# Kernel optimization log

Measured on AMD Instinct MI355X. Metric: run time of the kernel, lower is better.

## Reference

```python
import jax, jax.numpy as jnp
import numpy as np

B, S, H, NH, HD, ROT = 4, 1024, 2048, 16, 128, 64
P = NH * HD  # attention projection size = 2048
EPS = 1e-6


def setup_inputs() -> dict:
    key = jax.random.key(0)
    ks = jax.random.split(key, 12)
    T = B * S
    # rotary frequency table [max_pos=S, 1, ROT]
    inv_freq = 1.0 / (10000.0 ** (np.arange(0, ROT, 2, dtype=np.float32) / ROT))
    f = np.outer(np.arange(S, dtype=np.float32), inv_freq)  # [S, ROT/2]
    freqs = np.concatenate([f, f], axis=-1)[:, None, :].astype(np.float32)
    sc = 0.02
    return {
        "positions": jnp.tile(jnp.arange(S, dtype=jnp.int64), B),  # per-seq positions 0..S-1
        "hidden_states": jax.random.normal(ks[0], (T, H), jnp.float32),
        "rotary_pos_emb": jnp.asarray(freqs),
        "lf1_cache": jax.random.normal(ks[1], (B, 1, H), jnp.float32) * sc,
        "lf2_cache": jax.random.normal(ks[2], (B, 1, H // 2), jnp.float32) * sc,
        "Wqk": jax.random.normal(ks[3], (2 * P, H), jnp.float32) * sc,
        "Wv": jax.random.normal(ks[4], (P, H), jnp.float32) * sc,
        "Wo": jax.random.normal(ks[5], (H, P), jnp.float32) * sc,
        "conv1_w": jax.random.normal(ks[6], (H // 2, H, 2), jnp.float32) * sc,  # [out, in, tap]
        "conv1_b": jnp.zeros((H // 2,), jnp.float32),
        "conv2_w": jax.random.normal(ks[7], (H, H // 2, 2), jnp.float32) * sc,
        "conv2_b": jnp.zeros((H,), jnp.float32),
        "ln_g": jnp.ones((H,), jnp.float32),
    }


def reference(positions, hidden_states, rotary_pos_emb, lf1_cache, lf2_cache,
              Wqk, Wv, Wo, conv1_w, conv1_b, conv2_w, conv2_b, ln_g):
    T = hidden_states.shape[0]
    scaling = HD ** -0.5

    # v projection on raw hidden states (done before lf_gate in the source)
    v = hidden_states @ Wv.T  # [T, P]

    # ---- LocalizedFiltering (two causal 2-tap convs + residual + RMSNorm),
    # vectorized over all sequences (source loops per sequence) ----
    x = hidden_states.reshape(B, S, H)
    xc = jnp.concatenate([lf1_cache, x], axis=1)  # [B, S+1, H]
    o1 = (jnp.einsum('bsh,oh->bso', xc[:, :-1], conv1_w[..., 0])
          + jnp.einsum('bsh,oh->bso', xc[:, 1:], conv1_w[..., 1]) + conv1_b)  # [B,S,H/2]
    o1c = jnp.concatenate([lf2_cache, o1], axis=1)  # [B, S+1, H/2]
    o2 = (jnp.einsum('bsc,oc->bso', o1c[:, :-1], conv2_w[..., 0])
          + jnp.einsum('bsc,oc->bso', o1c[:, 1:], conv2_w[..., 1]) + conv2_b)  # [B,S,H]
    o3 = o2 + x
    lf = o3 * jax.lax.rsqrt(jnp.mean(o3 * o3, axis=-1, keepdims=True) + EPS) * ln_g

    hs = lf.reshape(T, H)
    qk = (hs @ Wqk.T).reshape(T, NH, 2 * HD)
    q, k = jnp.split(qk, 2, axis=-1)  # each [T, NH, HD]

    # partial rotary (mscale = 1.0 since use_yarn=False)
    f = rotary_pos_emb[positions]            # [T, 1, ROT]
    cos, sin = jnp.cos(f), jnp.sin(f)

    def rope(t):
        tr, tp = t[..., :ROT], t[..., ROT:]
        t1, t2 = jnp.split(tr, 2, axis=-1)
        rot = jnp.concatenate([-t2, t1], axis=-1)
        return jnp.concatenate([tr * cos + rot * sin, tp], axis=-1)

    qb = rope(q).reshape(B, S, NH, HD)
    kb = rope(k).reshape(B, S, NH, HD)
    vb = v.reshape(B, S, NH, HD)

    # causal attention per sequence
    scores = jnp.einsum('bqhd,bkhd->bhqk', qb, kb) * scaling
    mask = jnp.tril(jnp.ones((S, S), bool))
    scores = jnp.where(mask, scores, jnp.finfo(scores.dtype).min)
    attn = jax.nn.softmax(scores, axis=-1)
    out = jnp.einsum('bhqk,bkhd->bqhd', attn, vb).reshape(T, P)
    return out @ Wo.T  # [T, H]
```

## Files before the change

### kernel.cpp

```cpp
#include <hip/hip_runtime.h>

typedef __bf16 bf16;
typedef __bf16 bf16x8 __attribute__((ext_vector_type(8)));
typedef __bf16 bf16x4 __attribute__((ext_vector_type(4)));
typedef float f32x4 __attribute__((ext_vector_type(4)));
typedef float f32x2 __attribute__((ext_vector_type(2)));

#define DEVI __device__ __forceinline__

constexpr int Bc = 4, Sc = 1024, Hc = 2048, NHc = 16, HDc = 128;
constexpr int Tc = Bc * Sc;
constexpr int Pc = NHc * HDc;

DEVI void async16(const void* g, void* l) {
  __builtin_amdgcn_global_load_lds(
      (const __attribute__((address_space(1))) unsigned int*)g,
      (__attribute__((address_space(3))) unsigned int*)l, 16, 0, 0);
}

#define BAR() __builtin_amdgcn_s_barrier()
#define LGKM0()                                          \
  do {                                                   \
    asm volatile("s_waitcnt lgkmcnt(0)" ::: "memory");   \
    __builtin_amdgcn_sched_barrier(0);                   \
  } while (0)
#define VM0() asm volatile("s_waitcnt vmcnt(0)" ::: "memory")

template <int WM, int WN, int MREP, int NREP, int EPI>
__global__ __launch_bounds__(512, 2) void gemm8(
    const bf16* __restrict__ A, const bf16* __restrict__ W,
    void* __restrict__ C0, void* __restrict__ C1,
    const float* __restrict__ biasf, const f32x2* __restrict__ cst,
    int M, int N, int K) {
  constexpr int BM = WM * MREP * 16;
  constexpr int BN = WN * NREP * 16;
  constexpr int MH = MREP / 2, NH = NREP / 2;
  constexpr int LA = BM / 128;
  constexpr int LB = BN / 128;
  constexpr int STG = (BM + BN) * 128;
  constexpr int OUTB = (EPI == 3) ? 4 : 2;
  constexpr int CBYTES = BM * BN * OUTB;
  constexpr int LDSB = (2 * STG > CBYTES) ? 2 * STG : CBYTES;
  __shared__ char lds[LDSB];

  const int nbx = N / BN;
  const int nwg = (M / BM) * nbx;
  const int wgid = (blockIdx.x & 7) * (nwg >> 3) + (blockIdx.x >> 3);
  const int bx = wgid % nbx, by = wgid / nbx;
  const int m0 = by * BM, n0 = bx * BN;
  const int tid = threadIdx.x;
  const int w = tid >> 6, l = tid & 63;
  const int wm = w / WN, wn = w % WN;
  const int lr = l & 15, hi = l >> 4;

  auto vminf = [&] {
    constexpr int LL = LA + LB;
    if constexpr (LL == 4)      asm volatile("s_waitcnt vmcnt(4)" ::: "memory");
    else if constexpr (LL == 3) asm volatile("s_waitcnt vmcnt(3)" ::: "memory");
    else if constexpr (LL == 2) asm volatile("s_waitcnt vmcnt(2)" ::: "memory");
    else                        asm volatile("s_waitcnt vmcnt(0)" ::: "memory");
  };

  auto stageA = [&](int buf, int t, int half) {
#pragma unroll
    for (int c = 0; c < LA; ++c) {
      const int ch = c * 512 + tid;
      const int row = half * (BM / 2) + (ch >> 3);
      const int grp = ch & 7;
      async16(A + (size_t)(m0 + row) * K + (t << 6) + ((grp ^ (row & 7)) << 3),
              &lds[buf * STG + row * 128 + grp * 16]);
    }
  };
  auto stageB = [&](int buf, int t, int half) {
#pragma unroll
    for (int c = 0; c < LB; ++c) {
      const int ch = c * 512 + tid;
      const int row = half * (BN / 2) + (ch >> 3);
      const int grp = ch & 7;
      async16(W + (size_t)(n0 + row) * K + (t << 6) + ((grp ^ (row & 7)) << 3),
              &lds[buf * STG + BM * 128 + row * 128 + grp * 16]);
    }
  };
  auto LD = [&](const char* Lp, int row, int g) -> bf16x8 {
    return *(const bf16x8*)(Lp + ((size_t)row << 7) + ((g ^ (row & 7)) << 4));
  };

#define QUAD(MB_, NB_, FB_)                                                     \
  do {                                                                          \
    __builtin_amdgcn_s_setprio(1);                                              \
    _Pragma("unroll") for (int m = 0; m < MH; ++m)                              \
      _Pragma("unroll") for (int n = 0; n < NH; ++n)                            \
        _Pragma("unroll") for (int kk = 0; kk < 2; ++kk)                        \
          acc[(MB_) + m][(NB_) + n] = __builtin_amdgcn_mfma_f32_16x16x32_bf16(  \
              fa[m][kk], FB_[n][kk], acc[(MB_) + m][(NB_) + n], 0, 0, 0);       \
    __builtin_amdgcn_s_setprio(0);                                              \
  } while (0)

  f32x4 acc[MREP][NREP] = {};
  bf16x8 fa[MH][2], fb0[NH][2], fb1[NH][2];
  const int nk = K >> 6;

  stageA(0, 0, 0);
  stageB(0, 0, 0);
  stageA(0, 0, 1);
  stageB(0, 0, 1);
  stageA(1, 1, 0);
  stageB(1, 1, 0);
  vminf();
  BAR();

#pragma unroll 1
  for (int t = 0; t < nk; ++t) {
    const char* Lb = &lds[(t & 1) * STG];
    const int cur = t & 1, nbuf = cur ^ 1;
    const bool pf1 = (t + 1 < nk);
#pragma unroll
    for (int m = 0; m < MH; ++m) {
      const int r = wm * (MREP * 16) + m * 16 + lr;
      fa[m][0] = LD(Lb, r, hi);
      fa[m][1] = LD(Lb, r, 4 + hi);
    }
#pragma unroll
    for (int n = 0; n < NH; ++n) {
      const int r = BM + wn * (NREP * 16) + n * 16 + lr;
      fb0[n][0] = LD(Lb, r, hi);
      fb0[n][1] = LD(Lb, r, 4 + hi);
    }
    if (pf1) stageA(nbuf, t + 1, 1);
    BAR();
    LGKM0();
    QUAD(0, 0, fb0);
    BAR();
#pragma unroll
    for (int n = 0; n < NH; ++n) {
      const int r = BM + wn * (NREP * 16) + (NH + n) * 16 + lr;
      fb1[n][0] = LD(Lb, r, hi);
      fb1[n][1] = LD(Lb, r, 4 + hi);
    }
    if (pf1) stageB(nbuf, t + 1, 1);
    BAR();
    LGKM0();
    QUAD(0, NH, fb1);
    BAR();
#pragma unroll
    for (int m = 0; m < MH; ++m) {
      const int r = wm * (MREP * 16) + (MH + m) * 16 + lr;
      fa[m][0] = LD(Lb, r, hi);
      fa[m][1] = LD(Lb, r, 4 + hi);
    }
    BAR();
    LGKM0();
    QUAD(MH, NH, fb1);
    BAR();
    QUAD(MH, 0, fb0);
    if (t + 2 < nk) {
      stageA(cur, t + 2, 0);
      stageB(cur, t + 2, 0);
      vminf();
    } else {
      VM0();
    }
    BAR();
  }
#undef QUAD

  if constexpr (EPI == 0) {
    bf16* cl = (bf16*)lds;
#pragma unroll
    for (int mi = 0; mi < MREP; ++mi)
#pragma unroll
      for (int ni = 0; ni < NREP; ++ni) {
        const int col = wn * (NREP * 16) + ni * 16 + lr;
        const float bv = biasf ? biasf[n0 + col] : 0.f;
#pragma unroll
        for (int j = 0; j < 4; ++j) {
          const int row = wm * (MREP * 16) + mi * 16 + (hi << 2) + j;
          cl[row * BN + ((((col >> 3) ^ (row & 7)) << 3) | (col & 7))] =
              (bf16)(acc[mi][ni][j] + bv);
        }
      }
    __syncthreads();
    constexpr int GPR = BN / 8;
    constexpr int PT = BM * GPR / 512;
#pragma unroll
    for (int c = 0; c < PT; ++c) {
      const int ch = c * 512 + tid;
      const int row = ch / GPR, g = ch % GPR;
      bf16x8 vv = *(const bf16x8*)&cl[row * BN + ((g ^ (row & 7)) << 3)];
      *(bf16x8*)&((bf16*)C0)[(size_t)(m0 + row) * N + n0 + g * 8] = vv;
    }
  } else if constexpr (EPI == 1) {
    bf16* cl = (bf16*)lds;
#pragma unroll
    for (int mi = 0; mi < MREP; ++mi)
#pragma unroll
      for (int ni = 0; ni < NREP; ++ni) {
        const int col = wn * (NREP * 16) + ni * 16 + lr;
#pragma unroll
        for (int j = 0; j < 4; ++j) {
          const int row = wm * (MREP * 16) + mi * 16 + (hi << 2) + j;
          cl[col * BM + ((((row >> 3) ^ (col & 7)) << 3) | (row & 7))] =
              (bf16)acc[mi][ni][j];
        }
      }
    __syncthreads();
    const int s0 = m0 & 1023, bq = m0 >> 10;
    bf16* vT = (bf16*)C0;
    const size_t vbase = (((size_t)(bq * 16 + (n0 >> 7)) * 128) << 10) + s0;
    constexpr int GPR = BM / 8;
    constexpr int PT = BN * GPR / 512;
#pragma unroll
    for (int c = 0; c < PT; ++c) {
      const int ch = c * 512 + tid;
      const int d = ch / GPR, g = ch % GPR;
      bf16x8 vv = *(const bf16x8*)&cl[d * BM + ((g ^ (d & 7)) << 3)];
      *(bf16x8*)&vT[vbase + ((size_t)d << 10) + g * 8] = vv;
    }
  } else if constexpr (EPI == 2) {
    bf16* cl = (bf16*)lds;
#pragma unroll
    for (int mi = 0; mi < MREP; ++mi)
#pragma unroll
      for (int ni = 0; ni < NREP; ++ni) {
        const int col = wn * (NREP * 16) + ni * 16 + lr;
#pragma unroll
        for (int j = 0; j < 4; ++j) {
          const int row = wm * (MREP * 16) + mi * 16 + (hi << 2) + j;
          cl[row * BN + ((((col >> 3) ^ (row & 7)) << 3) | (col & 7))] =
              (bf16)acc[mi][ni][j];
        }
      }
    __syncthreads();
    const int s0 = m0 & 1023, bq = m0 >> 10, head = n0 >> 8;
    bf16* qr = (bf16*)C0;
    bf16* kr = (bf16*)C1;
    const size_t qbase = ((size_t)((bq * 16 + head) * 1024 + s0) << 7);
    constexpr int GPR = BN / 8;
    constexpr int PT = BM * GPR / 512;
#pragma unroll
    for (int c = 0; c < PT; ++c) {
      const int ch = c * 512 + tid;
      const int row = ch / GPR, g = ch % GPR;
      const int cc = g * 8;
      const int isk = cc >> 7, dd = cc & 127;
      bf16x8 vv = *(const bf16x8*)&cl[row * BN + ((g ^ (row & 7)) << 3)];
      bf16x8 out;
      if (dd < 64) {
        bf16x8 pp = *(const bf16x8*)&cl[row * BN + (((g ^ 4) ^ (row & 7)) << 3)];
        const f32x2* cp = &cst[(s0 + row) * 64 + dd];
#pragma unroll
        for (int e = 0; e < 8; ++e) {
          const f32x2 cs = cp[e];
          const float pv = (dd < 32) ? -(float)pp[e] : (float)pp[e];
          out[e] = (bf16)((float)vv[e] * cs[0] + pv * cs[1]);
        }
      } else {
        out = vv;
      }
      bf16* dst = isk ? kr : qr;
      *(bf16x8*)&dst[qbase + ((size_t)row << 7) + dd] = out;
    }
  } else {
    float* cl = (float*)lds;
#pragma unroll
    for (int mi = 0; mi < MREP; ++mi)
#pragma unroll
      for (int ni = 0; ni < NREP; ++ni) {
        const int col = wn * (NREP * 16) + ni * 16 + lr;
        const float bv = biasf ? biasf[n0 + col] : 0.f;
#pragma unroll
        for (int j = 0; j < 4; ++j) {
          const int row = wm * (MREP * 16) + mi * 16 + (hi << 2) + j;
          cl[row * BN + ((((col >> 2) ^ (row & 7)) << 2) | (col & 3))] =
              acc[mi][ni][j] + bv;
        }
      }
    __syncthreads();
    constexpr int GPR = BN / 4;
    constexpr int PT = BM * GPR / 512;
#pragma unroll
    for (int c = 0; c < PT; ++c) {
      const int ch = c * 512 + tid;
      const int row = ch / GPR, g = ch % GPR;
      f32x4 vv = *(const f32x4*)&cl[row * BN + ((g ^ (row & 7)) << 2)];
      *(f32x4*)&((float*)C0)[(size_t)(m0 + row) * N + n0 + g * 4] = vv;
    }
  }
}

template <int WM, int WN, int MREP, int NREP>
__global__ __launch_bounds__(WM * WN * 64, 2) void gemm_pipe(
    const bf16* __restrict__ A, const bf16* __restrict__ W, void* __restrict__ Cout,
    const float* __restrict__ bias, int M, int N, int K) {
  constexpr int BM = WM * MREP * 16;
  constexpr int BN = WN * NREP * 16;
  constexpr int THREADS = WM * WN * 64;
  constexpr int ROWS = BM + BN;
  constexpr int CHA = BM * 4 / THREADS;
  constexpr int CHB = BN * 4 / THREADS;
  static_assert(CHA + CHB == 4, "vmcnt ledger assumes 4 loads/thread/stage");
  __shared__ bf16 lds[4][ROWS * 32];
  static_assert(BM * BN * 2 <= sizeof(lds), "C tile must fit LDS for epilogue");

  const int nbx = N / BN;
  const int nwg = (M / BM) * nbx;
  const int wgid = (blockIdx.x & 7) * (nwg >> 3) + (blockIdx.x >> 3);
  const int bx = wgid % nbx, by = wgid / nbx;
  const int m0 = by * BM, n0 = bx * BN;
  const int tid = threadIdx.x;
  const int w = tid >> 6, l = tid & 63;
  const int wm = w / WN, wn = w % WN;
  const int lr = l & 15;
  const int hi = l >> 4;

  auto stage = [&](int slot, int t) {
    const int k0 = t << 5;
#pragma unroll
    for (int c = 0; c < CHA; ++c) {
      const int ch = c * THREADS + tid;
      const int row = ch >> 2, cg = ch & 3;
      const int gc = (cg ^ ((row >> 1) & 3)) << 3;
      async16(A + (size_t)(m0 + row) * K + k0 + gc, (char*)&lds[slot][0] + ch * 16);
    }
#pragma unroll
    for (int c = 0; c < CHB; ++c) {
      const int ch = c * THREADS + tid;
      const int row = ch >> 2, cg = ch & 3;
      const int gc = (cg ^ ((row >> 1) & 3)) << 3;
      async16(W + (size_t)(n0 + row) * K + k0 + gc,
              (char*)&lds[slot][0] + (BM * 4 + ch) * 16);
    }
  };

  f32x4 acc[MREP][NREP] = {};
  const int nk = K >> 5;

  stage(0, 0);
  stage(1, 1);
  stage(2, 2);
  asm volatile("s_waitcnt vmcnt(8)" ::: "memory");
  __builtin_amdgcn_s_barrier();
  __builtin_amdgcn_sched_barrier(0);

  bf16x8 fAc[MREP], fBc[NREP], fAn[MREP], fBn[NREP];
  {
    const char* nb = (const char*)&lds[0][0];
#pragma unroll
    for (int mi = 0; mi < MREP; ++mi) {
      const int r = wm * (MREP * 16) + mi * 16 + lr;
      fAc[mi] = *(const bf16x8*)(nb + r * 64 + ((hi ^ ((r >> 1) & 3)) << 4));
    }
#pragma unroll
    for (int ni = 0; ni < NREP; ++ni) {
      const int r = BM + wn * (NREP * 16) + ni * 16 + lr;
      fBc[ni] = *(const bf16x8*)(nb + r * 64 + ((hi ^ ((r >> 1) & 3)) << 4));
    }
  }

#define GSTEP(T_, CA, CB, NA, NB)                                              \
  do {                                                                         \
    if ((T_) + 2 < nk) asm volatile("s_waitcnt vmcnt(4)" ::: "memory");        \
    else               asm volatile("s_waitcnt vmcnt(0)" ::: "memory");        \
    __builtin_amdgcn_s_barrier();                                              \
    __builtin_amdgcn_sched_barrier(0);                                         \
    if ((T_) + 3 < nk) stage(((T_) + 3) & 3, (T_) + 3);                        \
    if ((T_) + 1 < nk) {                                                       \
      const char* nb = (const char*)&lds[((T_) + 1) & 3][0];                   \
      _Pragma("unroll") for (int mi = 0; mi < MREP; ++mi) {                    \
        const int r = wm * (MREP * 16) + mi * 16 + lr;                         \
        NA[mi] = *(const bf16x8*)(nb + r * 64 + ((hi ^ ((r >> 1) & 3)) << 4)); \
      }                                                                        \
      _Pragma("unroll") for (int ni = 0; ni < NREP; ++ni) {                    \
        const int r = BM + wn * (NREP * 16) + ni * 16 + lr;                    \
        NB[ni] = *(const bf16x8*)(nb + r * 64 + ((hi ^ ((r >> 1) & 3)) << 4)); \
      }                                                                        \
    }                                                                          \
    __builtin_amdgcn_s_setprio(1);                                             \
    _Pragma("unroll") for (int mi = 0; mi < MREP; ++mi)                        \
      _Pragma("unroll") for (int ni = 0; ni < NREP; ++ni)                      \
        acc[mi][ni] =                                                          \
            __builtin_amdgcn_mfma_f32_16x16x32_bf16(CA[mi], CB[ni], acc[mi][ni], 0, 0, 0); \
    __builtin_amdgcn_s_setprio(0);                                             \
  } while (0)

  for (int t = 0; t < nk; t += 2) {
    GSTEP(t, fAc, fBc, fAn, fBn);
    GSTEP(t + 1, fAn, fBn, fAc, fBc);
  }
#undef GSTEP

  __syncthreads();
  {
    bf16* cl = (bf16*)&lds[0][0];
#pragma unroll
    for (int mi = 0; mi < MREP; ++mi) {
#pragma unroll
      for (int ni = 0; ni < NREP; ++ni) {
        const int col = wn * (NREP * 16) + ni * 16 + lr;
        const float bv = bias ? bias[n0 + col] : 0.f;
#pragma unroll
        for (int j = 0; j < 4; ++j) {
          const int row = wm * (MREP * 16) + mi * 16 + (hi << 2) + j;
          cl[row * BN + ((((col >> 3) ^ (row & 7)) << 3) | (col & 7))] =
              (bf16)(acc[mi][ni][j] + bv);
        }
      }
    }
    __syncthreads();
    constexpr int GPR = BN / 8;
    constexpr int PT = BM * GPR / THREADS;
#pragma unroll
    for (int c = 0; c < PT; ++c) {
      const int ch = c * THREADS + tid;
      const int row = ch / GPR, g = ch % GPR;
      bf16x8 vv = *(const bf16x8*)&cl[row * BN + ((g ^ (row & 7)) << 3)];
      *(bf16x8*)&((bf16*)Cout)[(size_t)(m0 + row) * N + n0 + g * 8] = vv;
    }
  }
}

__global__ void k_f2b4(const float* __restrict__ in, bf16* __restrict__ out, int n4) {
  int i = blockIdx.x * 256 + threadIdx.x;
  if (i >= n4) return;
  float4 v = ((const float4*)in)[i];
  bf16x4 o = {(bf16)v.x, (bf16)v.y, (bf16)v.z, (bf16)v.w};
  ((bf16x4*)out)[i] = o;
}

__global__ void k_trig(const float* __restrict__ rot, f32x2* __restrict__ cst) {
  int i = blockIdx.x * 256 + threadIdx.x;
  float f = rot[i];
  f32x2 cs = {cosf(f), sinf(f)};
  cst[i] = cs;
}

__global__ void k_build_a1(const float* __restrict__ hid, const float* __restrict__ lf1,
                           bf16* __restrict__ hsb, bf16* __restrict__ A1) {
  int idx = blockIdx.x * 256 + threadIdx.x;
  int t = idx >> 11, h = idx & 2047;
  float x = hid[idx];
  hsb[idx] = (bf16)x;
  float xp;
  if ((t & (Sc - 1)) == 0)
    xp = lf1[(t >> 10) * Hc + h];
  else
    xp = hid[idx - Hc];
  size_t a = ((size_t)t << 12) + 2 * h;
  A1[a] = (bf16)xp;
  A1[a + 1] = (bf16)x;
}

__global__ void k_build_a2(const bf16* __restrict__ o1, const float* __restrict__ lf2,
                           bf16* __restrict__ A2) {
  int idx = blockIdx.x * 256 + threadIdx.x;
  int t = idx >> 10, c = idx & 1023;
  bf16 cur = o1[idx];
  bf16 prev;
  if ((t & (Sc - 1)) == 0)
    prev = (bf16)lf2[(t >> 10) * 1024 + c];
  else
    prev = o1[idx - 1024];
  size_t a = ((size_t)t << 11) + 2 * c;
  A2[a] = prev;
  A2[a + 1] = cur;
}

__global__ __launch_bounds__(256) void k_rmsnorm(const bf16* __restrict__ o2,
                                                 const float* __restrict__ hid,
                                                 const float* __restrict__ g,
                                                 bf16* __restrict__ lf) {
  int t = blockIdx.x, tid = threadIdx.x;
  size_t base = ((size_t)t << 11) + tid * 8;
  bf16x8 ov = *(const bf16x8*)&o2[base];
  const float* hp = &hid[base];
  float vals[8];
  float ss = 0.f;
#pragma unroll
  for (int i = 0; i < 8; ++i) {
    float x = (float)ov[i] + hp[i];
    vals[i] = x;
    ss += x * x;
  }
#pragma unroll
  for (int off = 1; off < 64; off <<= 1) ss += __shfl_xor(ss, off);
  __shared__ float red[4];
  if ((tid & 63) == 0) red[tid >> 6] = ss;
  __syncthreads();
  float tot = red[0] + red[1] + red[2] + red[3];
  float inv = rsqrtf(tot * (1.f / 2048.f) + 1e-6f);
  bf16x8 o;
#pragma unroll
  for (int i = 0; i < 8; ++i) o[i] = (bf16)(vals[i] * inv * g[tid * 8 + i]);
  *(bf16x8*)&lf[base] = o;
}

__global__ __launch_bounds__(256, 2) void k_attn(const bf16* __restrict__ qr,
                                                 const bf16* __restrict__ kr,
                                                 const bf16* __restrict__ vT,
                                                 bf16* __restrict__ att) {
  __shared__ bf16 Ks[2][64 * 128];
  __shared__ bf16 Vs[2][128 * 64];
  __shared__ bf16 plds[4][16 * 64];
  const int bid = blockIdx.x;
  const int xcd = bid & 7, jj = bid >> 3;
  const int bn = xcd * 8 + (jj >> 3);
  const int pr = jj & 7;
  const int tid = threadIdx.x, w = tid >> 6, l = tid & 63;
  const int lr = l & 15, hi = l >> 4;
  const bf16* kb = kr + ((size_t)bn << 17);
  const bf16* vb = vT + ((size_t)bn << 17);
  const int b = bn >> 4, hh = bn & 15;
  const float scaling = 0.08838834764831845f;

  auto stage = [&](int buf, int kt) {
#pragma unroll
    for (int c = 0; c < 4; ++c) {
      int chunk = c * 256 + tid;
      int prow = chunk >> 4, pcg = chunk & 15;
      async16(kb + ((size_t)(kt * 64 + prow) << 7) + ((pcg ^ (prow & 7)) << 3),
              (char*)&Ks[buf][0] + chunk * 16);
    }
#pragma unroll
    for (int c = 0; c < 4; ++c) {
      int chunk = c * 256 + tid;
      int prow = chunk >> 3, pcg = chunk & 7;
      async16(vb + ((size_t)prow << 10) + kt * 64 + ((pcg ^ (prow & 7)) << 3),
              (char*)&Vs[buf][0] + chunk * 16);
    }
  };

#pragma unroll 1
  for (int phase = 0; phase < 2; ++phase) {
    const int qt = phase ? (15 - pr) : pr;
    const int qg0 = qt * 64 + w * 16;
    const bf16* qb = qr + ((size_t)(bn * 1024 + qg0) << 7);
    bf16x8 qf[4];
#pragma unroll
    for (int ks = 0; ks < 4; ++ks) qf[ks] = *(const bf16x8*)&qb[lr * 128 + ks * 32 + hi * 8];
    f32x4 oacc[8] = {};
    float mrow[4] = {-1e30f, -1e30f, -1e30f, -1e30f};
    float lrow[4] = {0.f, 0.f, 0.f, 0.f};
    const int nkb = qt + 1;

    stage(0, 0);
    __syncthreads();

    for (int kbt = 0; kbt < nkb; ++kbt) {
      const int cur = kbt & 1;
      if (kbt + 1 < nkb) stage(cur ^ 1, kbt + 1);

      f32x4 sacc[4] = {};
#pragma unroll
      for (int n = 0; n < 4; ++n) {
        const int krow = n * 16 + lr;
#pragma unroll
        for (int ks = 0; ks < 4; ++ks) {
          bf16x8 kf = *(const bf16x8*)&Ks[cur][(krow << 7) + ((((ks << 2) | hi) ^ (krow & 7)) << 3)];
          sacc[n] = __builtin_amdgcn_mfma_f32_16x16x32_bf16(qf[ks], kf, sacc[n], 0, 0, 0);
        }
      }
      const bool needmask = (kbt * 64 + 63 > qg0);
#pragma unroll
      for (int n = 0; n < 4; ++n) {
        int kg = kbt * 64 + n * 16 + lr;
#pragma unroll
        for (int j = 0; j < 4; ++j) {
          float sv = sacc[n][j] * scaling;
          if (needmask && kg > qg0 + hi * 4 + j) sv = -1e30f;
          sacc[n][j] = sv;
        }
      }
      float sf[4];
#pragma unroll
      for (int j = 0; j < 4; ++j) {
        float pm = fmaxf(fmaxf(sacc[0][j], sacc[1][j]), fmaxf(sacc[2][j], sacc[3][j]));
        pm = fmaxf(pm, __shfl_xor(pm, 1));
        pm = fmaxf(pm, __shfl_xor(pm, 2));
        pm = fmaxf(pm, __shfl_xor(pm, 4));
        pm = fmaxf(pm, __shfl_xor(pm, 8));
        float mn = fmaxf(mrow[j], pm);
        sf[j] = __expf(mrow[j] - mn);
        mrow[j] = mn;
      }
#pragma unroll
      for (int n = 0; n < 4; ++n)
#pragma unroll
        for (int j = 0; j < 4; ++j) sacc[n][j] = __expf(sacc[n][j] - mrow[j]);
#pragma unroll
      for (int j = 0; j < 4; ++j) {
        float ps = sacc[0][j] + sacc[1][j] + sacc[2][j] + sacc[3][j];
        ps += __shfl_xor(ps, 1);
        ps += __shfl_xor(ps, 2);
        ps += __shfl_xor(ps, 4);
        ps += __shfl_xor(ps, 8);
        lrow[j] = lrow[j] * sf[j] + ps;
      }
#pragma unroll
      for (int dt = 0; dt < 8; ++dt)
#pragma unroll
        for (int j = 0; j < 4; ++j) oacc[dt][j] *= sf[j];
#pragma unroll
      for (int n = 0; n < 4; ++n)
#pragma unroll
        for (int j = 0; j < 4; ++j)
          plds[w][(hi * 4 + j) * 64 + n * 16 + lr] = (bf16)sacc[n][j];
      asm volatile("s_waitcnt lgkmcnt(0)" ::: "memory");
#pragma unroll
      for (int ks2 = 0; ks2 < 2; ++ks2) {
        bf16x8 pf = *(const bf16x8*)&plds[w][lr * 64 + ks2 * 32 + hi * 8];
#pragma unroll
        for (int dt = 0; dt < 8; ++dt) {
          const int vrow = dt * 16 + lr;
          bf16x8 vf = *(const bf16x8*)&Vs[cur][(vrow << 6) + ((((ks2 << 2) | hi) ^ (lr & 7)) << 3)];
          oacc[dt] = __builtin_amdgcn_mfma_f32_16x16x32_bf16(pf, vf, oacc[dt], 0, 0, 0);
        }
      }
      __syncthreads();
    }

#pragma unroll
    for (int j = 0; j < 4; ++j) {
      float inv = 1.f / lrow[j];
      int qg = qg0 + hi * 4 + j;
      size_t obase = ((size_t)(b * 1024 + qg) << 11) + hh * 128;
#pragma unroll
      for (int dt = 0; dt < 8; ++dt) att[obase + dt * 16 + lr] = (bf16)(oacc[dt][j] * inv);
    }
  }
}

extern "C" void kernel_launch(void* const* d_in, const int* in_sizes, int n_in,
                              void* d_out, int out_size, void* d_ws, size_t ws_size,
                              hipStream_t stream) {
  const float* hid = (const float*)d_in[1];
  const float* rot = (const float*)d_in[2];
  const float* lf1 = (const float*)d_in[3];
  const float* lf2 = (const float*)d_in[4];
  const float* Wqk = (const float*)d_in[5];
  const float* Wv  = (const float*)d_in[6];
  const float* Wo  = (const float*)d_in[7];
  const float* c1w = (const float*)d_in[8];
  const float* c1b = (const float*)d_in[9];
  const float* c2w = (const float*)d_in[10];
  const float* c2b = (const float*)d_in[11];
  const float* lng = (const float*)d_in[12];
  float* outp = (float*)d_out;
  char* ws = (char*)d_ws;

  const size_t MB = 1ull << 20;
  bf16* Wslot = (bf16*)(ws + 0 * MB);
  bf16* A1    = (bf16*)(ws + 16 * MB);
  bf16* qr    = (bf16*)(ws + 16 * MB);
  bf16* kr    = (bf16*)(ws + 32 * MB);
  bf16* hsb   = (bf16*)(ws + 48 * MB);
  bf16* lfb   = hsb;
  bf16* vT    = (bf16*)(ws + 64 * MB);
  bf16* o1    = (bf16*)(ws + 80 * MB);
  bf16* A2    = (bf16*)(ws + 88 * MB);
  bf16* att   = A2;
  bf16* o2    = (bf16*)(ws + 104 * MB);
  f32x2* cst  = (f32x2*)(ws + 120 * MB);

  auto f2b = [&](const float* in, bf16* out, int n) {
    int n4 = n / 4;
    k_f2b4<<<(n4 + 255) / 256, 256, 0, stream>>>(in, out, n4);
  };

  k_trig<<<Sc * 64 / 256, 256, 0, stream>>>(rot, cst);

  f2b(Wv, Wslot, 2048 * 2048);
  k_build_a1<<<Tc * Hc / 256, 256, 0, stream>>>(hid, lf1, hsb, A1);
  gemm8<4, 2, 4, 4, 1><<<256, 512, 0, stream>>>(hsb, Wslot, vT, nullptr, nullptr, nullptr,
                                                Tc, Pc, Hc);

  f2b(c1w, Wslot, 1024 * 2048 * 2);
  gemm_pipe<2, 2, 4, 4><<<256, 256, 0, stream>>>(A1, Wslot, o1, c1b, Tc, 1024, 4096);

  k_build_a2<<<Tc * 1024 / 256, 256, 0, stream>>>(o1, lf2, A2);
  f2b(c2w, Wslot, 2048 * 1024 * 2);
  gemm8<4, 2, 4, 4, 0><<<256, 512, 0, stream>>>(A2, Wslot, o2, nullptr, c2b, nullptr,
                                                Tc, 2048, 2048);

  k_rmsnorm<<<Tc, 256, 0, stream>>>(o2, hid, lng, lfb);

  f2b(Wqk, Wslot, 4096 * 2048);
  gemm8<2, 4, 8, 4, 2><<<256, 512, 0, stream>>>(lfb, Wslot, qr, kr, nullptr, cst,
                                                Tc, 4096, Hc);

  k_attn<<<Bc * NHc * 8, 256, 0, stream>>>(qr, kr, vT, att);

  f2b(Wo, Wslot, 2048 * 2048);
  gemm8<4, 2, 4, 4, 3><<<256, 512, 0, stream>>>(att, Wslot, outp, nullptr, nullptr, nullptr,
                                                Tc, 2048, 2048);
}
```

Before: 354.0 us.

## Read conv taps from padded activations instead of materialized interleaved im2col buffers

Removes the k_build_a1/k_build_a2 kernels that wrote interleaved [prev,cur] im2col copies. Activations are now stored in a per-sequence padded layout (S+1 rows with the cache row first), and the conv GEMMs address tap 0 and tap 1 as two K halves of shifted rows. Conv weights are de-interleaved into tap-major order to match. The first conv GEMM writes straight into the padded o1 buffer. A new XCD-aware tile mapping for 256-tile gemm8 grids is also added. This saves several large memory passes at the cost of more complex address arithmetic in the A loads.

```diff
diff --git a/kernel.cpp b/kernel.cpp
--- a/kernel.cpp
+++ b/kernel.cpp
@@ -3,6 +3,7 @@
 typedef __bf16 bf16;
 typedef __bf16 bf16x8 __attribute__((ext_vector_type(8)));
 typedef __bf16 bf16x4 __attribute__((ext_vector_type(4)));
+typedef __bf16 bf16x2 __attribute__((ext_vector_type(2)));
 typedef float f32x4 __attribute__((ext_vector_type(4)));
 typedef float f32x2 __attribute__((ext_vector_type(2)));
 
@@ -11,6 +12,7 @@
 constexpr int Bc = 4, Sc = 1024, Hc = 2048, NHc = 16, HDc = 128;
 constexpr int Tc = Bc * Sc;
 constexpr int Pc = NHc * HDc;
+constexpr int SP = Sc + 1;
 
 DEVI void async16(const void* g, void* l) {
   __builtin_amdgcn_global_load_lds(
@@ -26,7 +28,7 @@
   } while (0)
 #define VM0() asm volatile("s_waitcnt vmcnt(0)" ::: "memory")
 
-template <int WM, int WN, int MREP, int NREP, int EPI>
+template <int WM, int WN, int MREP, int NREP, int EPI, int AMODE>
 __global__ __launch_bounds__(512, 2) void gemm8(
     const bf16* __restrict__ A, const bf16* __restrict__ W,
     void* __restrict__ C0, void* __restrict__ C1,
@@ -45,8 +47,16 @@
 
   const int nbx = N / BN;
   const int nwg = (M / BM) * nbx;
-  const int wgid = (blockIdx.x & 7) * (nwg >> 3) + (blockIdx.x >> 3);
-  const int bx = wgid % nbx, by = wgid / nbx;
+  int bx, by;
+  if (nwg == 256 && nbx == 16) {
+    const int xcd = blockIdx.x & 7, loc = blockIdx.x >> 3;
+    by = (xcd >> 1) * 4 + (loc >> 3);
+    bx = (xcd & 1) * 8 + (loc & 7);
+  } else {
+    const int wgid = (blockIdx.x & 7) * (nwg >> 3) + (blockIdx.x >> 3);
+    bx = wgid % nbx;
+    by = wgid / nbx;
+  }
   const int m0 = by * BM, n0 = bx * BN;
   const int tid = threadIdx.x;
   const int w = tid >> 6, l = tid & 63;
@@ -61,13 +71,27 @@
     else                        asm volatile("s_waitcnt vmcnt(0)" ::: "memory");
   };
 
+  auto aAddr = [&](int row, int t) -> const bf16* {
+    const int m = m0 + row;
+    if constexpr (AMODE == 0) {
+      return A + (size_t)m * K + (t << 6);
+    } else if constexpr (AMODE == 1) {
+      return A + (size_t)((m >> 10) * SP + (m & 1023) + 1) * K + (t << 6);
+    } else {
+      const int Kh2 = K >> 1, nkh = Kh2 >> 6;
+      const int tap = (t >= nkh) ? 1 : 0;
+      return A + (size_t)((m >> 10) * SP + (m & 1023) + tap) * Kh2 +
+             ((t - (tap ? nkh : 0)) << 6);
+    }
+  };
+
   auto stageA = [&](int buf, int t, int half) {
 #pragma unroll
     for (int c = 0; c < LA; ++c) {
       const int ch = c * 512 + tid;
       const int row = half * (BM / 2) + (ch >> 3);
       const int grp = ch & 7;
-      async16(A + (size_t)(m0 + row) * K + (t << 6) + ((grp ^ (row & 7)) << 3),
+      async16(aAddr(row, t) + ((grp ^ (row & 7)) << 3),
               &lds[buf * STG + row * 128 + grp * 16]);
     }
   };
@@ -288,7 +312,7 @@
   }
 }
 
-template <int WM, int WN, int MREP, int NREP>
+template <int WM, int WN, int MREP, int NREP, int AMODE, bool OUTPAD>
 __global__ __launch_bounds__(WM * WN * 64, 2) void gemm_pipe(
     const bf16* __restrict__ A, const bf16* __restrict__ W, void* __restrict__ Cout,
     const float* __restrict__ bias, int M, int N, int K) {
@@ -313,6 +337,18 @@
   const int lr = l & 15;
   const int hi = l >> 4;
 
+  auto aAddr = [&](int row, int t) -> const bf16* {
+    const int m = m0 + row;
+    if constexpr (AMODE == 2) {
+      const int Kh2 = K >> 1, nkh = Kh2 >> 5;
+      const int tap = (t >= nkh) ? 1 : 0;
+      return A + (size_t)((m >> 10) * SP + (m & 1023) + tap) * Kh2 +
+             ((t - (tap ? nkh : 0)) << 5);
+    } else {
+      return A + (size_t)m * K + (t << 5);
+    }
+  };
+
   auto stage = [&](int slot, int t) {
     const int k0 = t << 5;
 #pragma unroll
@@ -320,7 +356,7 @@
       const int ch = c * THREADS + tid;
       const int row = ch >> 2, cg = ch & 3;
       const int gc = (cg ^ ((row >> 1) & 3)) << 3;
-      async16(A + (size_t)(m0 + row) * K + k0 + gc, (char*)&lds[slot][0] + ch * 16);
+      async16(aAddr(row, t) + gc, (char*)&lds[slot][0] + ch * 16);
     }
 #pragma unroll
     for (int c = 0; c < CHB; ++c) {
@@ -413,8 +449,11 @@
     for (int c = 0; c < PT; ++c) {
       const int ch = c * THREADS + tid;
       const int row = ch / GPR, g = ch % GPR;
+      const int mr = m0 + row;
+      const size_t orow = OUTPAD ? (size_t)((mr >> 10) * SP + (mr & 1023) + 1)
+                                 : (size_t)mr;
       bf16x8 vv = *(const bf16x8*)&cl[row * BN + ((g ^ (row & 7)) << 3)];
-      *(bf16x8*)&((bf16*)Cout)[(size_t)(m0 + row) * N + n0 + g * 8] = vv;
+      *(bf16x8*)&((bf16*)Cout)[orow * N + n0 + g * 8] = vv;
     }
   }
 }
@@ -427,6 +466,18 @@
   ((bf16x4*)out)[i] = o;
 }
 
+__global__ void k_deint(const float* __restrict__ in, bf16* __restrict__ out,
+                        int O, int Hd) {
+  int i = blockIdx.x * 256 + threadIdx.x;
+  if (i >= O * (Hd >> 1)) return;
+  int o = i / (Hd >> 1), h0 = (i % (Hd >> 1)) * 2;
+  float4 v = *(const float4*)&in[(size_t)o * Hd * 2 + h0 * 2];
+  bf16x2 t0 = {(bf16)v.x, (bf16)v.z};
+  bf16x2 t1 = {(bf16)v.y, (bf16)v.w};
+  *(bf16x2*)&out[(size_t)o * 2 * Hd + h0] = t0;
+  *(bf16x2*)&out[(size_t)o * 2 * Hd + Hd + h0] = t1;
+}
+
 __global__ void k_trig(const float* __restrict__ rot, f32x2* __restrict__ cst) {
   int i = blockIdx.x * 256 + threadIdx.x;
   float f = rot[i];
@@ -434,35 +485,21 @@
   cst[i] = cs;
 }
 
-__global__ void k_build_a1(const float* __restrict__ hid, const float* __restrict__ lf1,
-                           bf16* __restrict__ hsb, bf16* __restrict__ A1) {
+__global__ void k_build_hsbp(const float* __restrict__ hid, const float* __restrict__ lf1,
+                             const float* __restrict__ lf2,
+                             bf16* __restrict__ hsbp, bf16* __restrict__ o1p) {
   int idx = blockIdx.x * 256 + threadIdx.x;
   int t = idx >> 11, h = idx & 2047;
-  float x = hid[idx];
-  hsb[idx] = (bf16)x;
-  float xp;
-  if ((t & (Sc - 1)) == 0)
-    xp = lf1[(t >> 10) * Hc + h];
-  else
-    xp = hid[idx - Hc];
-  size_t a = ((size_t)t << 12) + 2 * h;
-  A1[a] = (bf16)xp;
-  A1[a + 1] = (bf16)x;
-}
-
-__global__ void k_build_a2(const bf16* __restrict__ o1, const float* __restrict__ lf2,
-                           bf16* __restrict__ A2) {
-  int idx = blockIdx.x * 256 + threadIdx.x;
-  int t = idx >> 10, c = idx & 1023;
-  bf16 cur = o1[idx];
-  bf16 prev;
-  if ((t & (Sc - 1)) == 0)
-    prev = (bf16)lf2[(t >> 10) * 1024 + c];
-  else
-    prev = o1[idx - 1024];
-  size_t a = ((size_t)t << 11) + 2 * c;
-  A2[a] = prev;
-  A2[a + 1] = cur;
+  int b = t >> 10, s = t & 1023;
+  hsbp[((size_t)(b * SP + s + 1) << 11) + h] = (bf16)hid[idx];
+  if (idx < Bc * Hc) {
+    int bb = idx >> 11, hh = idx & 2047;
+    hsbp[((size_t)(bb * SP) << 11) + hh] = (bf16)lf1[idx];
+  }
+  if (idx < Bc * 1024) {
+    int bb = idx >> 10, cc = idx & 1023;
+    o1p[((size_t)(bb * SP) << 10) + cc] = (bf16)lf2[idx];
+  }
 }
 
 __global__ __launch_bounds__(256) void k_rmsnorm(const bf16* __restrict__ o2,
@@ -649,17 +686,15 @@
 
   const size_t MB = 1ull << 20;
   bf16* Wslot = (bf16*)(ws + 0 * MB);
-  bf16* A1    = (bf16*)(ws + 16 * MB);
-  bf16* qr    = (bf16*)(ws + 16 * MB);
-  bf16* kr    = (bf16*)(ws + 32 * MB);
-  bf16* hsb   = (bf16*)(ws + 48 * MB);
-  bf16* lfb   = hsb;
-  bf16* vT    = (bf16*)(ws + 64 * MB);
-  bf16* o1    = (bf16*)(ws + 80 * MB);
-  bf16* A2    = (bf16*)(ws + 88 * MB);
-  bf16* att   = A2;
-  bf16* o2    = (bf16*)(ws + 104 * MB);
-  f32x2* cst  = (f32x2*)(ws + 120 * MB);
+  bf16* hsbp  = (bf16*)(ws + 16 * MB);
+  bf16* att   = (bf16*)(ws + 16 * MB);
+  bf16* o1p   = (bf16*)(ws + 34 * MB);
+  bf16* o2    = (bf16*)(ws + 43 * MB);
+  bf16* lfb   = (bf16*)(ws + 59 * MB);
+  bf16* vT    = (bf16*)(ws + 75 * MB);
+  bf16* qr    = (bf16*)(ws + 91 * MB);
+  bf16* kr    = (bf16*)(ws + 107 * MB);
+  f32x2* cst  = (f32x2*)(ws + 123 * MB);
 
   auto f2b = [&](const float* in, bf16* out, int n) {
     int n4 = n / 4;
@@ -667,29 +702,29 @@
   };
 
   k_trig<<<Sc * 64 / 256, 256, 0, stream>>>(rot, cst);
+  k_build_hsbp<<<Tc * Hc / 256, 256, 0, stream>>>(hid, lf1, lf2, hsbp, o1p);
 
   f2b(Wv, Wslot, 2048 * 2048);
-  k_build_a1<<<Tc * Hc / 256, 256, 0, stream>>>(hid, lf1, hsb, A1);
-  gemm8<4, 2, 4, 4, 1><<<256, 512, 0, stream>>>(hsb, Wslot, vT, nullptr, nullptr, nullptr,
-                                                Tc, Pc, Hc);
-
-  f2b(c1w, Wslot, 1024 * 2048 * 2);
-  gemm_pipe<2, 2, 4, 4><<<256, 256, 0, stream>>>(A1, Wslot, o1, c1b, Tc, 1024, 4096);
-
-  k_build_a2<<<Tc * 1024 / 256, 256, 0, stream>>>(o1, lf2, A2);
-  f2b(c2w, Wslot, 2048 * 1024 * 2);
-  gemm8<4, 2, 4, 4, 0><<<256, 512, 0, stream>>>(A2, Wslot, o2, nullptr, c2b, nullptr,
-                                                Tc, 2048, 2048);
+  gemm8<4, 2, 4, 4, 1, 1><<<256, 512, 0, stream>>>(hsbp, Wslot, vT, nullptr, nullptr,
+                                                   nullptr, Tc, Pc, Hc);
+
+  k_deint<<<(1024 * 1024 + 255) / 256, 256, 0, stream>>>(c1w, Wslot, 1024, 2048);
+  gemm_pipe<2, 2, 4, 4, 2, true><<<256, 256, 0, stream>>>(hsbp, Wslot, o1p, c1b,
+                                                          Tc, 1024, 4096);
+
+  k_deint<<<(2048 * 512 + 255) / 256, 256, 0, stream>>>(c2w, Wslot, 2048, 1024);
+  gemm8<4, 2, 4, 4, 0, 2><<<256, 512, 0, stream>>>(o1p, Wslot, o2, nullptr, c2b,
+                                                   nullptr, Tc, 2048, 2048);
 
   k_rmsnorm<<<Tc, 256, 0, stream>>>(o2, hid, lng, lfb);
 
   f2b(Wqk, Wslot, 4096 * 2048);
-  gemm8<2, 4, 8, 4, 2><<<256, 512, 0, stream>>>(lfb, Wslot, qr, kr, nullptr, cst,
-                                                Tc, 4096, Hc);
+  gemm8<2, 4, 8, 4, 2, 0><<<256, 512, 0, stream>>>(lfb, Wslot, qr, kr, nullptr, cst,
+                                                   Tc, 4096, Hc);
 
   k_attn<<<Bc * NHc * 8, 256, 0, stream>>>(qr, kr, vT, att);
 
   f2b(Wo, Wslot, 2048 * 2048);
-  gemm8<4, 2, 4, 4, 3><<<256, 512, 0, stream>>>(att, Wslot, outp, nullptr, nullptr, nullptr,
-                                                Tc, 2048, 2048);
-}
+  gemm8<4, 2, 4, 4, 3, 0><<<256, 512, 0, stream>>>(att, Wslot, outp, nullptr, nullptr,
+                                                   nullptr, Tc, 2048, 2048);
+}
```

After: 346.8 us. -2.0%, faster.
